# Optimization experiments

Measured on AMD Instinct MI355X. Metric: run time of the kernel, lower is better.

## Reference

```python
import jax, jax.numpy as jnp
import numpy as np

B, T, H, O = 256, 2048, 64, 2


def setup_inputs() -> dict:
    key = jax.random.key(0)
    ks = jax.random.split(key, 14)
    def lin(k, out_f, in_f):
        bound = np.sqrt(6.0 / (in_f + out_f))
        return jax.random.uniform(k, (out_f, in_f), jnp.float32, -bound, bound)
    return {
        "x": jax.random.normal(ks[0], (B, T, 2), jnp.float32),
        "h0": jax.random.normal(ks[1], (1, B, H), jnp.float32),
        "Wa": lin(ks[2], H, H + 1), "ba": jnp.zeros((H,), jnp.float32),
        "Wp1": lin(ks[3], H, H + 1), "bp1": jnp.zeros((H,), jnp.float32),
        "Wp2": lin(ks[4], H, H + 1), "bp2": jnp.zeros((H,), jnp.float32),
        "Wf": lin(ks[5], H, 2 * H), "bf": jnp.zeros((H,), jnp.float32),
        "Wg": lin(ks[6], H, 2 * H), "bg": jnp.zeros((H,), jnp.float32),
        "Wo": lin(ks[7], O, H), "bo": jnp.zeros((O,), jnp.float32),
    }


def reference(x, h0, Wa, ba, Wp1, bp1, Wp2, bp2, Wf, bf, Wg, bg, Wo, bo):
    # x: [B, T, 2] (I/Q), h0: [1, B, H]
    xt = jnp.swapaxes(x, 0, 1)  # [T, B, 2]

    def step(h, x_t):
        i = x_t[:, 0:1]
        q = x_t[:, 1:2]
        amp = jnp.sqrt(i * i + q * q)
        theta = jnp.arctan2(q, i)
        cos_t = jnp.cos(theta)
        sin_t = jnp.sin(theta)
        a = jnp.tanh(jnp.concatenate([h, amp], -1) @ Wa.T + ba)
        p1 = jnp.tanh(jnp.concatenate([h, cos_t], -1) @ Wp1.T + bp1)
        p2 = jnp.tanh(jnp.concatenate([h, sin_t], -1) @ Wp2.T + bp2)
        u = a * p1 * p2 * (1 - a) * (1 - p1) * (1 - p2)
        hu = jnp.concatenate([h, u], -1)
        f = jax.nn.sigmoid(hu @ Wf.T + bf)
        g = jnp.tanh(hu @ Wg.T + bg)
        h_new = f * h + (1 - f) * g
        y = h_new @ Wo.T + bo
        return h_new, y

    _, ys = jax.lax.scan(step, h0[0], xt)  # ys: [T, B, O]
    return jnp.swapaxes(ys, 0, 1)  # [B, T, O]
```

## Files before the change

### kernel.cpp

```cpp
#include <hip/hip_runtime.h>
#include <math.h>

#define BB 256
#define TT 2048
#define HH 64

typedef _Float16 half2v __attribute__((ext_vector_type(2)));
typedef __fp16  fp16v2 __attribute__((ext_vector_type(2)));
union H2I { half2v h; unsigned int i; };

#if __has_builtin(__builtin_amdgcn_rcpf)
__device__ __forceinline__ float fast_rcp(float v) { return __builtin_amdgcn_rcpf(v); }
#else
__device__ __forceinline__ float fast_rcp(float v) { return 1.0f / v; }
#endif
#if __has_builtin(__builtin_amdgcn_rsqf)
__device__ __forceinline__ float fast_rsq(float v) { return __builtin_amdgcn_rsqf(v); }
#else
__device__ __forceinline__ float fast_rsq(float v) { return rsqrtf(v); }
#endif

__device__ __forceinline__ float tanh_fast(float v) {
    float e = __expf(2.0f * v);
    return fmaf(-2.0f, fast_rcp(e + 1.0f), 1.0f);
}

__device__ __forceinline__ float sigmoid_fast(float v) {
    return fast_rcp(1.0f + __expf(-v));
}

__device__ __forceinline__ float fdot2(half2v a, half2v b, float c) {
    return __builtin_amdgcn_fdot2(a, b, c, false);
}

__device__ __forceinline__ half2v pack_pair(float a, float b) {
    fp16v2 r = __builtin_amdgcn_cvt_pkrtz(a, b);
    return __builtin_bit_cast(half2v, r);
}

__device__ __forceinline__ void pin_h2(half2v& v) {
    H2I u; u.h = v;
    asm volatile("" : "+v"(u.i));
    v = u.h;
}

__device__ __forceinline__ float dpp_neighbor(float v) {
    return __int_as_float(__builtin_amdgcn_mov_dpp(__float_as_int(v), 0xB1, 0xf, 0xf, true));
}

__device__ __forceinline__ half2v h2_from_u32(unsigned int w) {
    H2I u; u.i = w;
    return u.h;
}

__global__ __launch_bounds__(64, 1)
void pgjanet_kernel(const float* __restrict__ x,
                    const float* __restrict__ h0,
                    const float* __restrict__ Wa,  const float* __restrict__ ba,
                    const float* __restrict__ Wp1, const float* __restrict__ bp1,
                    const float* __restrict__ Wp2, const float* __restrict__ bp2,
                    const float* __restrict__ Wf,  const float* __restrict__ bf,
                    const float* __restrict__ Wg,  const float* __restrict__ bg,
                    const float* __restrict__ Wo,  const float* __restrict__ bo,
                    float* __restrict__ out)
{
    const int b = blockIdx.x;
    const int j = threadIdx.x;

    __shared__ float4 xt[TT];
    __shared__ float  hbuf[64][HH + 1];
    __shared__ float  woLDS[2 * HH];
    __shared__ __align__(16) unsigned int hpk[32];
    __shared__ __align__(16) unsigned int upk[32];

    for (int t = j; t < TT; t += 64) {
        float2 xi = reinterpret_cast<const float2*>(x)[(size_t)b * TT + t];
        float r2 = xi.x * xi.x + xi.y * xi.y;
        float rq = fast_rsq(r2);
        bool ok = r2 > 0.f;
        xt[t] = make_float4(ok ? r2 * rq : 0.f,
                            ok ? xi.x * rq : 1.f,
                            ok ? xi.y * rq : 0.f,
                            0.f);
    }
    for (int i = j; i < 2 * HH; i += 64) woLDS[i] = Wo[i];

    half2v w5[5][32], wfu[32], wgu[32];
    {
        const float* Wsrc[5] = {Wa, Wp1, Wp2, Wf, Wg};
        const int    ldv[5]  = {HH + 1, HH + 1, HH + 1, 2 * HH, 2 * HH};
#pragma unroll
        for (int g = 0; g < 5; ++g) {
            const float* r = Wsrc[g] + (size_t)j * ldv[g];
#pragma unroll
            for (int m = 0; m < 32; ++m) w5[g][m] = pack_pair(r[2 * m], r[2 * m + 1]);
        }
        const float* rf = Wf + (size_t)j * (2 * HH) + HH;
        const float* rg = Wg + (size_t)j * (2 * HH) + HH;
#pragma unroll
        for (int m = 0; m < 32; ++m) {
            wfu[m] = pack_pair(rf[2 * m], rf[2 * m + 1]);
            wgu[m] = pack_pair(rg[2 * m], rg[2 * m + 1]);
        }
#pragma unroll
        for (int g = 0; g < 5; ++g)
#pragma unroll
            for (int m = 0; m < 32; ++m) pin_h2(w5[g][m]);
#pragma unroll
        for (int m = 0; m < 32; ++m) { pin_h2(wfu[m]); pin_h2(wgu[m]); }
    }

    const float waX  = Wa [j * (HH + 1) + HH];
    const float wp1X = Wp1[j * (HH + 1) + HH];
    const float wp2X = Wp2[j * (HH + 1) + HH];
    const float ba_r = ba[j], bp1_r = bp1[j], bp2_r = bp2[j];
    const float bf_r = bf[j], bg_r = bg[j];
    const float bo0  = bo[0], bo1 = bo[1];

    float  h  = h0[b * HH + j];
    float* yp = out + (size_t)b * (TT * 2);

    __syncthreads();

    float4 xv = xt[0];

    for (int t = 0; t < TT; ++t) {
        const int tn = (t + 1 < TT) ? (t + 1) : t;
        float4 xv_n = xt[tn];

        {
            float hn = dpp_neighbor(h);
            H2I hp; hp.h = pack_pair(h, hn);
            if ((j & 1) == 0) hpk[j >> 1] = hp.i;
        }
        uint4 hw[8];
#pragma unroll
        for (int i = 0; i < 8; ++i) hw[i] = reinterpret_cast<const uint4*>(hpk)[i];

        float acc0 = fmaf(xv.x, waX,  ba_r);
        float acc1 = fmaf(xv.y, wp1X, bp1_r);
        float acc2 = fmaf(xv.z, wp2X, bp2_r);
        float acc3 = bf_r;
        float acc4 = bg_r;
#pragma unroll
        for (int i = 0; i < 8; ++i) {
#pragma unroll
            for (int q = 0; q < 4; ++q) {
                const int m = 4 * i + q;
                half2v s = h2_from_u32((&hw[i].x)[q]);
                acc0 = fdot2(s, w5[0][m], acc0);
                acc1 = fdot2(s, w5[1][m], acc1);
                acc2 = fdot2(s, w5[2][m], acc2);
                acc3 = fdot2(s, w5[3][m], acc3);
                acc4 = fdot2(s, w5[4][m], acc4);
            }
        }

        float av = tanh_fast(acc0);
        float p1 = tanh_fast(acc1);
        float p2 = tanh_fast(acc2);
        float u = fmaf(-av, av, av) * fmaf(-p1, p1, p1) * fmaf(-p2, p2, p2);

        {
            float un = dpp_neighbor(u);
            H2I up; up.h = pack_pair(u, un);
            if ((j & 1) == 0) upk[j >> 1] = up.i;
        }
        uint4 uw[8];
#pragma unroll
        for (int i = 0; i < 8; ++i) uw[i] = reinterpret_cast<const uint4*>(upk)[i];

        float f0 = acc3, f1 = 0.f, g0 = acc4, g1 = 0.f;
#pragma unroll
        for (int i = 0; i < 4; ++i) {
#pragma unroll
            for (int q = 0; q < 4; ++q) {
                const int m  = 4 * i + q;
                const int m2 = m + 16;
                half2v s0 = h2_from_u32((&uw[i].x)[q]);
                half2v s1 = h2_from_u32((&uw[i + 4].x)[q]);
                f0 = fdot2(s0, wfu[m],  f0);
                f1 = fdot2(s1, wfu[m2], f1);
                g0 = fdot2(s0, wgu[m],  g0);
                g1 = fdot2(s1, wgu[m2], g1);
            }
        }
        float f = sigmoid_fast(f0 + f1);
        float g = tanh_fast(g0 + g1);
        h = fmaf(f, h - g, g);

        hbuf[t & 63][j] = h;

        if ((t & 63) == 63) {
            float y0 = bo0, y1 = bo1;
#pragma unroll 4
            for (int k = 0; k < HH; ++k) {
                float hv = hbuf[j][k];
                y0 = fmaf(hv, woLDS[k],      y0);
                y1 = fmaf(hv, woLDS[HH + k], y1);
            }
            reinterpret_cast<float2*>(yp)[(t - 63) + j] = make_float2(y0, y1);
        }

        xv = xv_n;
    }
}

extern "C" void kernel_launch(void* const* d_in, const int* in_sizes, int n_in,
                              void* d_out, int out_size, void* d_ws, size_t ws_size,
                              hipStream_t stream) {
    const float* x   = (const float*)d_in[0];
    const float* h0  = (const float*)d_in[1];
    const float* Wa  = (const float*)d_in[2];
    const float* ba  = (const float*)d_in[3];
    const float* Wp1 = (const float*)d_in[4];
    const float* bp1 = (const float*)d_in[5];
    const float* Wp2 = (const float*)d_in[6];
    const float* bp2 = (const float*)d_in[7];
    const float* Wf  = (const float*)d_in[8];
    const float* bf  = (const float*)d_in[9];
    const float* Wg  = (const float*)d_in[10];
    const float* bg  = (const float*)d_in[11];
    const float* Wo  = (const float*)d_in[12];
    const float* bo  = (const float*)d_in[13];
    float* out = (float*)d_out;

    pgjanet_kernel<<<dim3(BB), dim3(64), 0, stream>>>(
        x, h0, Wa, ba, Wp1, bp1, Wp2, bp2, Wf, bf, Wg, bg, Wo, bo, out);
}
```

Measured before the change: 1.514 ms.

## Offload recurrent gate matvecs to MFMA with readlane broadcasts for the rest

The per-step matrix-vector products for the a/p1/p2 gates and the u-part of the f gate now run on MFMA 16x16x32 f16 instructions. The hidden vector is replicated across the M dimension and only row 0 of each output tile is kept. The h-part of f and g and the u-part of g stay on fdot2, with their operands now fed by readlane broadcasts instead of LDS reads. This aims to cut VALU dot-product work on the sequential critical path, at the cost of wasted MFMA rows, MFMA latency, many scalar readlanes and higher register pressure from the fragment layout.

Result: slower. 1.711 ms (+13.1%).

```diff
diff --git a/kernel.cpp b/kernel.cpp
--- a/kernel.cpp
+++ b/kernel.cpp
@@ -7,7 +7,10 @@
 
 typedef _Float16 half2v __attribute__((ext_vector_type(2)));
 typedef __fp16  fp16v2 __attribute__((ext_vector_type(2)));
+typedef _Float16 half8  __attribute__((ext_vector_type(8)));
+typedef float    f32x4  __attribute__((ext_vector_type(4)));
 union H2I { half2v h; unsigned int i; };
+union F8  { half8 h; uint4 u; };
 
 #if __has_builtin(__builtin_amdgcn_rcpf)
 __device__ __forceinline__ float fast_rcp(float v) { return __builtin_amdgcn_rcpf(v); }
@@ -24,33 +27,45 @@
     float e = __expf(2.0f * v);
     return fmaf(-2.0f, fast_rcp(e + 1.0f), 1.0f);
 }
-
 __device__ __forceinline__ float sigmoid_fast(float v) {
     return fast_rcp(1.0f + __expf(-v));
 }
-
 __device__ __forceinline__ float fdot2(half2v a, half2v b, float c) {
     return __builtin_amdgcn_fdot2(a, b, c, false);
 }
-
 __device__ __forceinline__ half2v pack_pair(float a, float b) {
     fp16v2 r = __builtin_amdgcn_cvt_pkrtz(a, b);
     return __builtin_bit_cast(half2v, r);
 }
-
+__device__ __forceinline__ unsigned pack_u32(float a, float b) {
+    fp16v2 r = __builtin_amdgcn_cvt_pkrtz(a, b);
+    return __builtin_bit_cast(unsigned, r);
+}
 __device__ __forceinline__ void pin_h2(half2v& v) {
     H2I u; u.h = v;
     asm volatile("" : "+v"(u.i));
     v = u.h;
 }
-
+__device__ __forceinline__ void pin_f8(half8& v) {
+    F8 f; f.h = v;
+    asm volatile("" : "+v"(f.u.x), "+v"(f.u.y), "+v"(f.u.z), "+v"(f.u.w));
+    v = f.h;
+}
+__device__ __forceinline__ half2v bcast_pair(half2v v, int lane) {
+    H2I u; u.h = v;
+    H2I w; w.i = __builtin_amdgcn_readlane(u.i, lane);
+    return w.h;
+}
 __device__ __forceinline__ float dpp_neighbor(float v) {
     return __int_as_float(__builtin_amdgcn_mov_dpp(__float_as_int(v), 0xB1, 0xf, 0xf, true));
 }
-
-__device__ __forceinline__ half2v h2_from_u32(unsigned int w) {
-    H2I u; u.i = w;
-    return u.h;
+__device__ __forceinline__ half8 make_frag(const float* p) {
+    F8 f;
+    f.u.x = pack_u32(p[0], p[1]);
+    f.u.y = pack_u32(p[2], p[3]);
+    f.u.z = pack_u32(p[4], p[5]);
+    f.u.w = pack_u32(p[6], p[7]);
+    return f.h;
 }
 
 __global__ __launch_bounds__(64, 1)
@@ -66,6 +81,8 @@
 {
     const int b = blockIdx.x;
     const int j = threadIdx.x;
+    const int c   = j & 15;
+    const int grp = j >> 4;
 
     __shared__ float4 xt[TT];
     __shared__ float  hbuf[64][HH + 1];
@@ -78,36 +95,51 @@
         float r2 = xi.x * xi.x + xi.y * xi.y;
         float rq = fast_rsq(r2);
         bool ok = r2 > 0.f;
-        xt[t] = make_float4(ok ? r2 * rq : 0.f,
-                            ok ? xi.x * rq : 1.f,
-                            ok ? xi.y * rq : 0.f,
-                            0.f);
+        xt[t] = make_float4(ok ? r2 * rq : 0.f, ok ? xi.x * rq : 1.f,
+                            ok ? xi.y * rq : 0.f, 0.f);
     }
     for (int i = j; i < 2 * HH; i += 64) woLDS[i] = Wo[i];
 
-    half2v w5[5][32], wfu[32], wgu[32];
+    half8 WB[3][4][2];
+    half8 UBf[4][2];
     {
-        const float* Wsrc[5] = {Wa, Wp1, Wp2, Wf, Wg};
-        const int    ldv[5]  = {HH + 1, HH + 1, HH + 1, 2 * HH, 2 * HH};
-#pragma unroll
-        for (int g = 0; g < 5; ++g) {
-            const float* r = Wsrc[g] + (size_t)j * ldv[g];
-#pragma unroll
-            for (int m = 0; m < 32; ++m) w5[g][m] = pack_pair(r[2 * m], r[2 * m + 1]);
-        }
-        const float* rf = Wf + (size_t)j * (2 * HH) + HH;
-        const float* rg = Wg + (size_t)j * (2 * HH) + HH;
+        const float* WsrcA[3] = {Wa, Wp1, Wp2};
+#pragma unroll
+        for (int g = 0; g < 3; ++g)
+#pragma unroll
+            for (int tau = 0; tau < 4; ++tau)
+#pragma unroll
+                for (int kt = 0; kt < 2; ++kt)
+                    WB[g][tau][kt] = make_frag(WsrcA[g] + (size_t)(16 * tau + c) * (HH + 1) + 32 * kt + grp * 8);
+#pragma unroll
+        for (int tau = 0; tau < 4; ++tau)
+#pragma unroll
+            for (int kt = 0; kt < 2; ++kt)
+                UBf[tau][kt] = make_frag(Wf + (size_t)(16 * tau + c) * (2 * HH) + HH + 32 * kt + grp * 8);
+#pragma unroll
+        for (int g = 0; g < 3; ++g)
+#pragma unroll
+            for (int tau = 0; tau < 4; ++tau)
+#pragma unroll
+                for (int kt = 0; kt < 2; ++kt) pin_f8(WB[g][tau][kt]);
+#pragma unroll
+        for (int tau = 0; tau < 4; ++tau)
+#pragma unroll
+            for (int kt = 0; kt < 2; ++kt) pin_f8(UBf[tau][kt]);
+    }
+
+    half2v wfh[32], wgh[32], wgu[32];
+    {
+        const float* rf = Wf + (size_t)j * (2 * HH);
+        const float* rg = Wg + (size_t)j * (2 * HH);
 #pragma unroll
         for (int m = 0; m < 32; ++m) {
-            wfu[m] = pack_pair(rf[2 * m], rf[2 * m + 1]);
-            wgu[m] = pack_pair(rg[2 * m], rg[2 * m + 1]);
-        }
-#pragma unroll
-        for (int g = 0; g < 5; ++g)
-#pragma unroll
-            for (int m = 0; m < 32; ++m) pin_h2(w5[g][m]);
-#pragma unroll
-        for (int m = 0; m < 32; ++m) { pin_h2(wfu[m]); pin_h2(wgu[m]); }
+            wfh[m] = pack_pair(rf[2 * m], rf[2 * m + 1]);
+            wgh[m] = pack_pair(rg[2 * m], rg[2 * m + 1]);
+            wgu[m] = pack_pair(rg[HH + 2 * m], rg[HH + 2 * m + 1]);
+        }
+#pragma unroll
+        for (int m = 0; m < 32; ++m) { pin_h2(wfh[m]); pin_h2(wgh[m]); pin_h2(wgu[m]); }
     }
 
     const float waX  = Wa [j * (HH + 1) + HH];
@@ -122,71 +154,91 @@
 
     __syncthreads();
 
+    const bool b4 = (j & 16) != 0, b5 = (j & 32) != 0;
+    const f32x4 zz = {0.f, 0.f, 0.f, 0.f};
     float4 xv = xt[0];
 
     for (int t = 0; t < TT; ++t) {
         const int tn = (t + 1 < TT) ? (t + 1) : t;
         float4 xv_n = xt[tn];
 
+        float hn = dpp_neighbor(h);
+        half2v hp = pack_pair(h, hn);
         {
-            float hn = dpp_neighbor(h);
-            H2I hp; hp.h = pack_pair(h, hn);
-            if ((j & 1) == 0) hpk[j >> 1] = hp.i;
-        }
-        uint4 hw[8];
-#pragma unroll
-        for (int i = 0; i < 8; ++i) hw[i] = reinterpret_cast<const uint4*>(hpk)[i];
-
-        float acc0 = fmaf(xv.x, waX,  ba_r);
-        float acc1 = fmaf(xv.y, wp1X, bp1_r);
-        float acc2 = fmaf(xv.z, wp2X, bp2_r);
-        float acc3 = bf_r;
-        float acc4 = bg_r;
-#pragma unroll
-        for (int i = 0; i < 8; ++i) {
-#pragma unroll
-            for (int q = 0; q < 4; ++q) {
-                const int m = 4 * i + q;
-                half2v s = h2_from_u32((&hw[i].x)[q]);
-                acc0 = fdot2(s, w5[0][m], acc0);
-                acc1 = fdot2(s, w5[1][m], acc1);
-                acc2 = fdot2(s, w5[2][m], acc2);
-                acc3 = fdot2(s, w5[3][m], acc3);
-                acc4 = fdot2(s, w5[4][m], acc4);
+            H2I w_; w_.h = hp;
+            if ((j & 1) == 0) hpk[j >> 1] = w_.i;
+        }
+        F8 a0u, a1u;
+        a0u.u = *reinterpret_cast<const uint4*>(&hpk[grp * 4]);
+        a1u.u = *reinterpret_cast<const uint4*>(&hpk[16 + grp * 4]);
+
+        float F0 = bf_r, F1 = 0.f, G0 = bg_r, G1 = 0.f;
+#pragma unroll
+        for (int m = 0; m < 16; ++m) {
+            half2v s0 = bcast_pair(hp, 2 * m);
+            half2v s1 = bcast_pair(hp, 2 * (m + 16));
+            F0 = fdot2(s0, wfh[m],      F0);
+            F1 = fdot2(s1, wfh[m + 16], F1);
+            G0 = fdot2(s0, wgh[m],      G0);
+            G1 = fdot2(s1, wgh[m + 16], G1);
+        }
+        float accF = F0 + F1;
+        float accG = G0 + G1;
+
+        half8 hA0 = a0u.h, hA1 = a1u.h;
+        f32x4 accA[3][4];
+#pragma unroll
+        for (int g = 0; g < 3; ++g)
+#pragma unroll
+            for (int tau = 0; tau < 4; ++tau) {
+                accA[g][tau] = __builtin_amdgcn_mfma_f32_16x16x32_f16(hA0, WB[g][tau][0], zz, 0, 0, 0);
+                accA[g][tau] = __builtin_amdgcn_mfma_f32_16x16x32_f16(hA1, WB[g][tau][1], accA[g][tau], 0, 0, 0);
             }
-        }
-
-        float av = tanh_fast(acc0);
-        float p1 = tanh_fast(acc1);
-        float p2 = tanh_fast(acc2);
+
+        float pre[3];
+#pragma unroll
+        for (int g = 0; g < 3; ++g) {
+            float s01 = b4 ? accA[g][1][0] : accA[g][0][0];
+            float s23 = b4 ? accA[g][3][0] : accA[g][2][0];
+            pre[g] = b5 ? s23 : s01;
+        }
+        float av = tanh_fast(pre[0] + fmaf(xv.x, waX,  ba_r));
+        float p1 = tanh_fast(pre[1] + fmaf(xv.y, wp1X, bp1_r));
+        float p2 = tanh_fast(pre[2] + fmaf(xv.z, wp2X, bp2_r));
         float u = fmaf(-av, av, av) * fmaf(-p1, p1, p1) * fmaf(-p2, p2, p2);
 
+        float un = dpp_neighbor(u);
+        half2v up = pack_pair(u, un);
         {
-            float un = dpp_neighbor(u);
-            H2I up; up.h = pack_pair(u, un);
-            if ((j & 1) == 0) upk[j >> 1] = up.i;
-        }
-        uint4 uw[8];
-#pragma unroll
-        for (int i = 0; i < 8; ++i) uw[i] = reinterpret_cast<const uint4*>(upk)[i];
-
-        float f0 = acc3, f1 = 0.f, g0 = acc4, g1 = 0.f;
-#pragma unroll
-        for (int i = 0; i < 4; ++i) {
-#pragma unroll
-            for (int q = 0; q < 4; ++q) {
-                const int m  = 4 * i + q;
-                const int m2 = m + 16;
-                half2v s0 = h2_from_u32((&uw[i].x)[q]);
-                half2v s1 = h2_from_u32((&uw[i + 4].x)[q]);
-                f0 = fdot2(s0, wfu[m],  f0);
-                f1 = fdot2(s1, wfu[m2], f1);
-                g0 = fdot2(s0, wgu[m],  g0);
-                g1 = fdot2(s1, wgu[m2], g1);
-            }
-        }
-        float f = sigmoid_fast(f0 + f1);
-        float g = tanh_fast(g0 + g1);
+            H2I w_; w_.h = up;
+            if ((j & 1) == 0) upk[j >> 1] = w_.i;
+        }
+        F8 u0u, u1u;
+        u0u.u = *reinterpret_cast<const uint4*>(&upk[grp * 4]);
+        u1u.u = *reinterpret_cast<const uint4*>(&upk[16 + grp * 4]);
+
+        float Gu0 = accG, Gu1 = 0.f;
+#pragma unroll
+        for (int m = 0; m < 16; ++m) {
+            half2v s0 = bcast_pair(up, 2 * m);
+            half2v s1 = bcast_pair(up, 2 * (m + 16));
+            Gu0 = fdot2(s0, wgu[m],      Gu0);
+            Gu1 = fdot2(s1, wgu[m + 16], Gu1);
+        }
+
+        half8 uA0 = u0u.h, uA1 = u1u.h;
+        f32x4 accCf[4];
+#pragma unroll
+        for (int tau = 0; tau < 4; ++tau) {
+            accCf[tau] = __builtin_amdgcn_mfma_f32_16x16x32_f16(uA0, UBf[tau][0], zz, 0, 0, 0);
+            accCf[tau] = __builtin_amdgcn_mfma_f32_16x16x32_f16(uA1, UBf[tau][1], accCf[tau], 0, 0, 0);
+        }
+        float fs01 = b4 ? accCf[1][0] : accCf[0][0];
+        float fs23 = b4 ? accCf[3][0] : accCf[2][0];
+        float fu   = b5 ? fs23 : fs01;
+
+        float f = sigmoid_fast(accF + fu);
+        float g = tanh_fast(Gu0 + Gu1);
         h = fmaf(f, h - g, g);
 
         hbuf[t & 63][j] = h;
```
